# Performance work log

Measured on AMD Instinct MI355X. Metric: run time of the kernel, lower is better.

## Reference

```python
import jax, jax.numpy as jnp
import numpy as np

B = 131072   # batch_sz
NB = 3       # n_blocks (n_agents)
SS = 16      # single_state
NA = 9       # n_action
VD = 128     # vector_dim
CM = 10      # confidence_mid_dim
EPS = 1e-8   # torch CosineSimilarity eps


def _linear_params(k, out_d, in_d):
    bound = 1.0 / np.sqrt(in_d)
    kw, kb = jax.random.split(k)
    W = jax.random.uniform(kw, (out_d, in_d), minval=-bound, maxval=bound, dtype=jnp.float32)
    b = jax.random.uniform(kb, (out_d,), minval=-bound, maxval=bound, dtype=jnp.float32)
    return W, b


def setup_inputs() -> dict:
    key = jax.random.key(0)
    ks = jax.random.split(key, 11)
    Wq, bq = _linear_params(ks[0], VD, SS + NA)
    Wk, bk = _linear_params(ks[1], VD, SS + NA)
    Wv, bv = _linear_params(ks[2], VD, SS + NA)
    W1, b1 = _linear_params(ks[3], VD, VD)
    W2, b2 = _linear_params(ks[4], SS, VD)
    Wc1, bc1 = _linear_params(ks[5], CM, NB * (SS + NA))
    Wc2, bc2 = _linear_params(ks[6], 3, CM)
    states = jax.random.normal(ks[7], (B, NB, SS), dtype=jnp.float32)
    action = jax.random.normal(ks[8], (B, NA), dtype=jnp.float32)
    block_id = jax.random.randint(ks[9], (B, NB), 0, 2, dtype=jnp.int32)
    return {
        'states': states, 'action': action, 'block_id': block_id,
        'Wq': Wq, 'bq': bq, 'Wk': Wk, 'bk': bk, 'Wv': Wv, 'bv': bv,
        'W1': W1, 'b1': b1, 'W2': W2, 'b2': b2,
        'Wc1': Wc1, 'bc1': bc1, 'Wc2': Wc2, 'bc2': bc2,
    }


def reference(states, action, block_id, Wq, bq, Wk, bk, Wv, bv, W1, b1, W2, b2, Wc1, bc1, Wc2, bc2):
    # create_block_action: broadcast action over blocks, mask non-selected blocks to -1
    act = jnp.where(block_id[:, :, None] == 1, action[:, None, :], -1.0)  # [B,NB,NA]
    ba = jnp.concatenate([states, act], axis=-1)                          # [B,NB,SS+NA]

    # QKV projections (fused over blocks instead of per-block loop)
    q = ba @ Wq.T + bq   # [B,NB,VD]
    k = ba @ Wk.T + bk
    v = ba @ Wv.T + bv

    # cosine-similarity attention: d[b,i,j] = cos(q[b,i], k[b,j])
    num = jnp.einsum('bid,bjd->bij', q, k)                                # [B,NB,NB]
    qn = jnp.linalg.norm(q, axis=-1)                                      # [B,NB]
    kn = jnp.linalg.norm(k, axis=-1)
    d = num / jnp.maximum(qn[:, :, None] * kn[:, None, :], EPS)
    a = jax.nn.softmax(d, axis=2)

    res = jnp.einsum('bij,bjd->bid', a, v)                                # [B,NB,VD]
    res = jnp.tanh(res @ W1.T + b1)
    res = res @ W2.T + b2                                                 # [B,NB,SS]
    res = res.reshape(B, 1, NB * SS)

    flat = ba.reshape(B, 1, NB * (SS + NA))                               # [B,1,75]
    conf = jax.nn.sigmoid(jax.nn.sigmoid(flat @ Wc1.T + bc1) @ Wc2.T + bc2)  # [B,1,3]

    residuals = jnp.concatenate([res, conf], axis=-1)                     # [B,1,51]
    base = jnp.concatenate(
        [states.reshape(B, 1, NB * SS), jnp.zeros((B, 1, 3), dtype=states.dtype)], axis=-1)
    return base + residuals
```

## Files before the change

kernel.cpp:

```cpp
#include <hip/hip_runtime.h>
#include <math.h>

#define BTOT 131072
#define NBK 3
#define SS 16
#define NA 9
#define BAD 25
#define STR 28
#define VD 128
#define CM 10
#define OUTD 51
#define EPS 1e-8f

#define O_GQK  0
#define O_GQQ  700
#define O_GKK  1400
#define O_V1   2100
#define O_V2   2128
#define O_VQ   2156
#define O_VK   2184
#define O_C    2212
#define O_M    2216
#define O_B2   7976
#define O_WC1  7992
#define O_BC1  8832
#define O_WC2  8844
#define O_BC2  8880
#define LDS_F  8884
#define O_PKM  LDS_F
#define O_PKW2 (LDS_F + 2048)
#define PKM_N  4096
#define PKW2_N 2048

#define NDOT  (O_M + PKM_N)
#define NCOPY (16 + 840 + 12 + 36 + 4 + PKW2_N)

typedef __attribute__((ext_vector_type(8))) short short8;
typedef __attribute__((ext_vector_type(4))) float floatx4;

__device__ __forceinline__ float fast_sigmoid(float x) {
    return __builtin_amdgcn_rcpf(1.0f + __expf(-x));
}

__device__ __forceinline__ unsigned short f2bf(float f) {
    unsigned int u = __float_as_uint(f);
    u += 0x7FFFu + ((u >> 16) & 1u);
    return (unsigned short)(u >> 16);
}

__global__ __launch_bounds__(256) void prep_dots(
    const float* __restrict__ Wq, const float* __restrict__ bq,
    const float* __restrict__ Wk, const float* __restrict__ bk,
    const float* __restrict__ Wv, const float* __restrict__ bv,
    const float* __restrict__ W1, const float* __restrict__ b1,
    float* __restrict__ ws) {
    int lane = threadIdx.x & 63;
    int gidx = blockIdx.x * 4 + (threadIdx.x >> 6);
    if (gidx >= NDOT) return;

    const float* pa = bq;  const float* pb = bk;
    int sa = 1, sb = 1;
    float scale = 1.0f, bias = 0.0f;
    bool zero = false;
    bool isbf = false; int bfpos = 0;

    if (gidx < O_M) {
        int idx = gidx;
        if (idx < O_GQQ) {
            int e = idx / STR, f = idx % STR;
            if (f < BAD) { pa = Wq + e; sa = BAD; pb = Wk + f; sb = BAD; }
            else zero = true;
        } else if (idx < O_GKK) {
            int j = idx - O_GQQ; int e = j / STR, f = j % STR;
            if (f < BAD && f <= e) { pa = Wq + e; sa = BAD; pb = Wq + f; sb = BAD; scale = (f == e) ? 1.0f : 2.0f; }
            else zero = true;
        } else if (idx < O_V1) {
            int j = idx - O_GKK; int e = j / STR, f = j % STR;
            if (f < BAD && f <= e) { pa = Wk + e; sa = BAD; pb = Wk + f; sb = BAD; scale = (f == e) ? 1.0f : 2.0f; }
            else zero = true;
        } else if (idx < O_V2) {
            int e = idx - O_V1;
            if (e < BAD) { pa = Wq + e; sa = BAD; pb = bk; }
            else zero = true;
        } else if (idx < O_VQ) {
            int e = idx - O_V2;
            if (e < BAD) { pa = Wk + e; sa = BAD; pb = bq; }
            else zero = true;
        } else if (idx < O_VK) {
            int e = idx - O_VQ;
            if (e < BAD) { pa = Wq + e; sa = BAD; pb = bq; }
            else zero = true;
        } else if (idx < O_C) {
            int e = idx - O_VK;
            if (e < BAD) { pa = Wk + e; sa = BAD; pb = bk; }
            else zero = true;
        } else {
            int j = idx - O_C;
            if (j == 0)      { pa = bq; pb = bk; }
            else if (j == 1) { pa = bq; pb = bq; }
            else if (j == 2) { pa = bk; pb = bk; }
            else zero = true;
        }
    } else {
        int p = gidx - O_M;
        isbf = true; bfpos = p;
        int l2 = (p >> 3) & 63, j = p & 7;
        int n = (p >> 9) * 16 + (l2 & 15);
        int k = ((l2 >> 4) << 3) + j;
        if (k < BAD)       { pa = W1 + n * VD; pb = Wv + k; sb = BAD; scale = 2.0f; }
        else if (k == BAD) { pa = W1 + n * VD; pb = bv; scale = 2.0f; bias = 2.0f * b1[n]; }
        else zero = true;
    }

    float s = 0.0f;
    if (!zero)
        s = pa[sa * lane] * pb[sb * lane] + pa[sa * (lane + 64)] * pb[sb * (lane + 64)];
    #pragma unroll
    for (int off = 1; off < 64; off <<= 1) s += __shfl_xor(s, off);
    float val = zero ? 0.0f : (s * scale + bias);
    if (lane == 0) {
        if (isbf) ((unsigned short*)(ws + O_PKM))[bfpos] = f2bf(val);
        else ws[gidx] = val;
    }
}

__global__ __launch_bounds__(256) void prep_copy(
    const float* __restrict__ W2, const float* __restrict__ b2,
    const float* __restrict__ Wc1, const float* __restrict__ bc1,
    const float* __restrict__ Wc2, const float* __restrict__ bc2,
    float* __restrict__ ws) {
    int c = blockIdx.x * 256 + threadIdx.x;
    if (c >= NCOPY) return;
    if (c < 16) { ws[O_B2 + c] = b2[c]; return; }
    c -= 16;
    if (c < 840) {
        int m = c / 84, r = c % 84, i = r / STR, f = r % STR;
        ws[O_WC1 + c] = (f < BAD) ? Wc1[m * (NBK * BAD) + i * BAD + f] : 0.0f;
        return;
    }
    c -= 840;
    if (c < 12) { ws[O_BC1 + c] = (c < CM) ? bc1[c] : 0.0f; return; }
    c -= 12;
    if (c < 36) { int o = c / 12, mm = c % 12; ws[O_WC2 + c] = (mm < CM) ? Wc2[o * CM + mm] : 0.0f; return; }
    c -= 36;
    if (c < 4) { ws[O_BC2 + c] = (c < 3) ? bc2[c] : 0.0f; return; }
    c -= 4;
    int kt = c >> 9, l = (c >> 3) & 63, j = c & 7;
    int o = l & 15;
    int k = kt * 32 + ((l >> 4) << 3) + j;
    ((unsigned short*)(ws + O_PKW2))[c] = f2bf(W2[o * VD + k]);
}

__global__ __launch_bounds__(256) void main_kernel(
    const float* __restrict__ states, const float* __restrict__ action,
    const int* __restrict__ block_id,
    const float* __restrict__ ws, float* __restrict__ out) {
    __shared__ __align__(16) unsigned short At[384 * 40];

    int t = threadIdx.x;
    int lane = t & 63;
    int h = t & 1;
    int le = t >> 1;
    long elem = (long)blockIdx.x * 128 + le;

    const float* st = states + elem * (NBK * SS);
    const float* ac = action + elem * NA;
    const int* bid = block_id + elem * NBK;

    float ba[NBK * BAD];
    #pragma unroll
    for (int i = 0; i < NBK; ++i) {
        const float4* s4 = (const float4*)(st + i * SS);
        #pragma unroll
        for (int w4 = 0; w4 < 4; ++w4) {
            float4 v = s4[w4];
            ba[i * BAD + w4 * 4 + 0] = v.x;
            ba[i * BAD + w4 * 4 + 1] = v.y;
            ba[i * BAD + w4 * 4 + 2] = v.z;
            ba[i * BAD + w4 * 4 + 3] = v.w;
        }
        bool sel = (bid[i] == 1);
        #pragma unroll
        for (int c = 0; c < NA; ++c)
            ba[i * BAD + SS + c] = sel ? ac[c] : -1.0f;
    }

    {
        const float* wc = ws + O_WC1 + h * 5 * 84;
        const float* bc = ws + O_BC1 + h * 5;
        float hp[5];
        #pragma unroll
        for (int k = 0; k < 5; ++k) {
            float s = bc[k];
            #pragma unroll
            for (int i = 0; i < NBK; ++i)
                #pragma unroll
                for (int f = 0; f < BAD; ++f)
                    s += wc[k * 84 + i * STR + f] * ba[i * BAD + f];
            hp[k] = fast_sigmoid(s);
        }
        float op5[5];
        #pragma unroll
        for (int k = 0; k < 5; ++k) op5[k] = __shfl_xor(hp[k], 1);
        if (h == 0) {
            float* op = out + elem * OUTD;
            #pragma unroll
            for (int o = 0; o < 3; ++o) {
                float s = ws[O_BC2 + o];
                #pragma unroll
                for (int m = 0; m < 5; ++m) s += ws[O_WC2 + o * 12 + m] * hp[m];
                #pragma unroll
                for (int m = 0; m < 5; ++m) s += ws[O_WC2 + o * 12 + 5 + m] * op5[m];
                op[48 + o] = fast_sigmoid(s);
            }
        }
    }

    float sl[NBK], dd[NBK];
    {
        const float* vA = ws + (h ? O_V2 : O_V1);
        const float* vB = ws + (h ? O_VK : O_VQ);
        #pragma unroll
        for (int p = 0; p < NBK; ++p) {
            float sA = 0.f, sB = 0.f;
            #pragma unroll
            for (int e = 0; e < BAD; ++e) {
                float b = ba[p * BAD + e];
                sA = fmaf(vA[e], b, sA);
                sB = fmaf(vB[e], b, sB);
            }
            sl[p] = sA; dd[p] = sB;
        }
    }

    float nm[NBK][NBK] = {{0.f,0.f,0.f},{0.f,0.f,0.f},{0.f,0.f,0.f}};
    {
        const float* gq = ws + O_GQK + h * STR;
        #pragma unroll
        for (int i13 = 0; i13 < 13; ++i13) {
            const float* grow = (i13 == 12) ? (ws + O_GQK + 24 * STR)
                                            : (gq + i13 * 2 * STR);
            float t0 = 0.f, t1 = 0.f, t2 = 0.f;
            #pragma unroll
            for (int f = 0; f < BAD; ++f) {
                float g = grow[f];
                t0 = fmaf(g, ba[0 * BAD + f], t0);
                t1 = fmaf(g, ba[1 * BAD + f], t1);
                t2 = fmaf(g, ba[2 * BAD + f], t2);
            }
            float zs = (i13 == 12) ? (1.0f - (float)h) : 1.0f;
            #pragma unroll
            for (int i = 0; i < NBK; ++i) {
                float be;
                if (i13 == 12) be = ba[i * BAD + 24] * zs;
                else {
                    float b_even = ba[i * BAD + 2 * i13];
                    float b_odd  = ba[i * BAD + 2 * i13 + 1];
                    be = h ? b_odd : b_even;
                }
                nm[i][0] = fmaf(be, t0, nm[i][0]);
                nm[i][1] = fmaf(be, t1, nm[i][1]);
                nm[i][2] = fmaf(be, t2, nm[i][2]);
            }
        }
        #pragma unroll
        for (int i = 0; i < NBK; ++i)
            #pragma unroll
            for (int j = 0; j < NBK; ++j)
                nm[i][j] += __shfl_xor(nm[i][j], 1);
    }

    float sn2[NBK] = {0.f, 0.f, 0.f};
    {
        const float* gt = ws + (h ? O_GKK : O_GQQ);
        #pragma unroll
        for (int e = 0; e < BAD; ++e) {
            float p0 = 0.f, p1 = 0.f, p2 = 0.f;
            #pragma unroll
            for (int f = 0; f <= e; ++f) {
                float g = gt[e * STR + f];
                p0 = fmaf(g, ba[0 * BAD + f], p0);
                p1 = fmaf(g, ba[1 * BAD + f], p1);
                p2 = fmaf(g, ba[2 * BAD + f], p2);
            }
            sn2[0] = fmaf(ba[0 * BAD + e], p0, sn2[0]);
            sn2[1] = fmaf(ba[1 * BAD + e], p1, sn2[1]);
            sn2[2] = fmaf(ba[2 * BAD + e], p2, sn2[2]);
        }
    }
    float c0 = ws[O_C + 0];
    float cc = ws[O_C + 1 + h];
    float rn[NBK];
    #pragma unroll
    for (int p = 0; p < NBK; ++p) {
        sn2[p] += 2.0f * dd[p] + cc;
        rn[p] = __builtin_amdgcn_sqrtf(fmaxf(sn2[p], 0.0f));
    }

    float orn[NBK], osl[NBK];
    #pragma unroll
    for (int p = 0; p < NBK; ++p) {
        orn[p] = __shfl_xor(rn[p], 1);
        osl[p] = __shfl_xor(sl[p], 1);
    }
    float s1v[NBK], s2v[NBK], qv[NBK], kv[NBK];
    #pragma unroll
    for (int p = 0; p < NBK; ++p) {
        s1v[p] = h ? osl[p] : sl[p];
        s2v[p] = h ? sl[p] : osl[p];
        qv[p]  = h ? orn[p] : rn[p];
        kv[p]  = h ? rn[p] : orn[p];
    }

    float att[NBK][NBK];
    #pragma unroll
    for (int i = 0; i < NBK; ++i) {
        float dv[NBK];
        #pragma unroll
        for (int j = 0; j < NBK; ++j)
            dv[j] = (nm[i][j] + s1v[i] + s2v[j] + c0) *
                    __builtin_amdgcn_rcpf(fmaxf(qv[i] * kv[j], EPS));
        float mx = fmaxf(dv[0], fmaxf(dv[1], dv[2]));
        float e0 = __expf(dv[0] - mx);
        float e1 = __expf(dv[1] - mx);
        float e2 = __expf(dv[2] - mx);
        float inv = __builtin_amdgcn_rcpf(e0 + e1 + e2);
        att[i][0] = e0 * inv;
        att[i][1] = e1 * inv;
        att[i][2] = e2 * inv;
    }

    #pragma unroll
    for (int i = 0; i < NBK; ++i) {
        unsigned int* dst = (unsigned int*)&At[(le * 3 + i) * 40];
        #pragma unroll
        for (int d = 0; d < 6; ++d) {
            float a_lo = ba[0 * BAD + 2 * d]     * att[i][0] + ba[1 * BAD + 2 * d]     * att[i][1] + ba[2 * BAD + 2 * d]     * att[i][2];
            float a_hi = ba[0 * BAD + 2 * d + 1] * att[i][0] + ba[1 * BAD + 2 * d + 1] * att[i][1] + ba[2 * BAD + 2 * d + 1] * att[i][2];
            float b_lo = ba[0 * BAD + 12 + 2 * d]     * att[i][0] + ba[1 * BAD + 12 + 2 * d]     * att[i][1] + ba[2 * BAD + 12 + 2 * d]     * att[i][2];
            float b_hi = ba[0 * BAD + 12 + 2 * d + 1] * att[i][0] + ba[1 * BAD + 12 + 2 * d + 1] * att[i][1] + ba[2 * BAD + 12 + 2 * d + 1] * att[i][2];
            float v_lo = h ? b_lo : a_lo;
            float v_hi = h ? b_hi : a_hi;
            dst[h * 6 + d] = (unsigned int)f2bf(v_lo) | ((unsigned int)f2bf(v_hi) << 16);
        }
        if (h) {
            float v24 = ba[0 * BAD + 24] * att[i][0] + ba[1 * BAD + 24] * att[i][1] + ba[2 * BAD + 24] * att[i][2];
            dst[12] = (unsigned int)f2bf(v24) | (0x3F80u << 16);
        } else {
            dst[13] = 0u; dst[14] = 0u; dst[15] = 0u;
        }
    }

    asm volatile("s_waitcnt lgkmcnt(0)" ::: "memory");

    {
        int w = t >> 6;
        int m = lane & 15, q = lane >> 4;
        const short8* pkM = (const short8*)(ws + O_PKM);
        const short8* pkW2 = (const short8*)(ws + O_PKW2);
        float b2v = ws[O_B2 + m];
        long blockbase = (long)blockIdx.x * 128;
        int addrA = ((q & 1) ? (m + 32) : m) << 2;
        int addrB = addrA + 64;
        bool hiSel = (q >= 2);

        for (int tt = 0; tt < 6; ++tt) {
            int tile = w * 6 + tt;
            short8 af = *(const short8*)&At[(tile * 16 + m) * 40 + q * 8];
            floatx4 accT[8];
            #pragma unroll
            for (int nt = 0; nt < 8; ++nt) {
                floatx4 z = {0.f, 0.f, 0.f, 0.f};
                accT[nt] = __builtin_amdgcn_mfma_f32_16x16x32_bf16(pkM[nt * 64 + lane], af, z, 0, 0, 0);
            }
            unsigned int pk[8][2];
            #pragma unroll
            for (int nt = 0; nt < 8; ++nt) {
                float x0 = fmaf(-2.0f, __builtin_amdgcn_rcpf(1.0f + __expf(accT[nt][0])), 1.0f);
                float x1 = fmaf(-2.0f, __builtin_amdgcn_rcpf(1.0f + __expf(accT[nt][1])), 1.0f);
                float x2 = fmaf(-2.0f, __builtin_amdgcn_rcpf(1.0f + __expf(accT[nt][2])), 1.0f);
                float x3 = fmaf(-2.0f, __builtin_amdgcn_rcpf(1.0f + __expf(accT[nt][3])), 1.0f);
                asm("v_cvt_pk_bf16_f32 %0, %1, %2" : "=v"(pk[nt][0]) : "v"(x0), "v"(x1));
                asm("v_cvt_pk_bf16_f32 %0, %1, %2" : "=v"(pk[nt][1]) : "v"(x2), "v"(x3));
            }
            floatx4 acc2 = {0.f, 0.f, 0.f, 0.f};
            #pragma unroll
            for (int kt = 0; kt < 4; ++kt) {
                int lo0 = __builtin_amdgcn_ds_bpermute(addrA, (int)pk[2 * kt][0]);
                int hi0 = __builtin_amdgcn_ds_bpermute(addrA, (int)pk[2 * kt + 1][0]);
                int lo1 = __builtin_amdgcn_ds_bpermute(addrA, (int)pk[2 * kt][1]);
                int hi1 = __builtin_amdgcn_ds_bpermute(addrA, (int)pk[2 * kt + 1][1]);
                int lo2 = __builtin_amdgcn_ds_bpermute(addrB, (int)pk[2 * kt][0]);
                int hi2 = __builtin_amdgcn_ds_bpermute(addrB, (int)pk[2 * kt + 1][0]);
                int lo3 = __builtin_amdgcn_ds_bpermute(addrB, (int)pk[2 * kt][1]);
                int hi3 = __builtin_amdgcn_ds_bpermute(addrB, (int)pk[2 * kt + 1][1]);
                union { unsigned int u[4]; short8 s; } a2u;
                a2u.u[0] = (unsigned int)(hiSel ? hi0 : lo0);
                a2u.u[1] = (unsigned int)(hiSel ? hi1 : lo1);
                a2u.u[2] = (unsigned int)(hiSel ? hi2 : lo2);
                a2u.u[3] = (unsigned int)(hiSel ? hi3 : lo3);
                acc2 = __builtin_amdgcn_mfma_f32_16x16x32_bf16(a2u.s, pkW2[kt * 64 + lane], acc2, 0, 0, 0);
            }
            #pragma unroll
            for (int rr = 0; rr < 4; ++rr) {
                int lrow = tile * 16 + q * 4 + rr;
                int et = lrow / 3, i = lrow - et * 3;
                long ge = blockbase + et;
                float base = states[ge * 48 + i * 16 + m];
                out[ge * OUTD + i * 16 + m] = acc2[rr] + base + b2v;
            }
        }
    }
}

extern "C" void kernel_launch(void* const* d_in, const int* in_sizes, int n_in,
                              void* d_out, int out_size, void* d_ws, size_t ws_size,
                              hipStream_t stream) {
    const float* states = (const float*)d_in[0];
    const float* action = (const float*)d_in[1];
    const int* block_id = (const int*)d_in[2];
    const float* Wq = (const float*)d_in[3];
    const float* bq = (const float*)d_in[4];
    const float* Wk = (const float*)d_in[5];
    const float* bk = (const float*)d_in[6];
    const float* Wv = (const float*)d_in[7];
    const float* bv = (const float*)d_in[8];
    const float* W1 = (const float*)d_in[9];
    const float* b1 = (const float*)d_in[10];
    const float* W2 = (const float*)d_in[11];
    const float* b2 = (const float*)d_in[12];
    const float* Wc1 = (const float*)d_in[13];
    const float* bc1 = (const float*)d_in[14];
    const float* Wc2 = (const float*)d_in[15];
    const float* bc2 = (const float*)d_in[16];
    float* out = (float*)d_out;
    float* ws = (float*)d_ws;

    hipLaunchKernelGGL(prep_dots, dim3((NDOT + 3) / 4), dim3(256), 0, stream,
                       Wq, bq, Wk, bk, Wv, bv, W1, b1, ws);
    hipLaunchKernelGGL(prep_copy, dim3((NCOPY + 255) / 256), dim3(256), 0, stream,
                       W2, b2, Wc1, bc1, Wc2, bc2, ws);
    hipLaunchKernelGGL(main_kernel, dim3(BTOT / 128), dim3(256), 0, stream,
                       states, action, block_id, ws, out);
}
```

Baseline: 167.8 us.

## Split element work across waves instead of lane pairs, exchange via LDS

Each element's two halves of work move from adjacent lanes to two different wavefronts. The half index is now wave-uniform, so branches are uniform and weight loads become scalar. Partial results that used to pass through shuffles now go through shared memory with block barriers. Blocks shrink to 128 threads covering 64 elements each, which adds LDS traffic and barriers and halves the per-block tile count.

```diff
diff --git a/kernel.cpp b/kernel.cpp
--- a/kernel.cpp
+++ b/kernel.cpp
@@ -151,17 +151,16 @@
     ((unsigned short*)(ws + O_PKW2))[c] = f2bf(W2[o * VD + k]);
 }
 
-__global__ __launch_bounds__(256) void main_kernel(
+__global__ __launch_bounds__(128) void main_kernel(
     const float* __restrict__ states, const float* __restrict__ action,
     const int* __restrict__ block_id,
     const float* __restrict__ ws, float* __restrict__ out) {
-    __shared__ __align__(16) unsigned short At[384 * 40];
+    __shared__ __align__(16) unsigned short At[192 * 40];
 
     int t = threadIdx.x;
     int lane = t & 63;
-    int h = t & 1;
-    int le = t >> 1;
-    long elem = (long)blockIdx.x * 128 + le;
+    int h_u = __builtin_amdgcn_readfirstlane(t >> 6);
+    long elem = (long)blockIdx.x * 64 + lane;
 
     const float* st = states + elem * (NBK * SS);
     const float* ac = action + elem * NA;
@@ -185,10 +184,10 @@
             ba[i * BAD + SS + c] = sel ? ac[c] : -1.0f;
     }
 
-    {
-        const float* wc = ws + O_WC1 + h * 5 * 84;
-        const float* bc = ws + O_BC1 + h * 5;
-        float hp[5];
+    float hp[5];
+    {
+        const float* wc = ws + O_WC1 + h_u * 5 * 84;
+        const float* bc = ws + O_BC1 + h_u * 5;
         #pragma unroll
         for (int k = 0; k < 5; ++k) {
             float s = bc[k];
@@ -199,27 +198,12 @@
                     s += wc[k * 84 + i * STR + f] * ba[i * BAD + f];
             hp[k] = fast_sigmoid(s);
         }
-        float op5[5];
-        #pragma unroll
-        for (int k = 0; k < 5; ++k) op5[k] = __shfl_xor(hp[k], 1);
-        if (h == 0) {
-            float* op = out + elem * OUTD;
-            #pragma unroll
-            for (int o = 0; o < 3; ++o) {
-                float s = ws[O_BC2 + o];
-                #pragma unroll
-                for (int m = 0; m < 5; ++m) s += ws[O_WC2 + o * 12 + m] * hp[m];
-                #pragma unroll
-                for (int m = 0; m < 5; ++m) s += ws[O_WC2 + o * 12 + 5 + m] * op5[m];
-                op[48 + o] = fast_sigmoid(s);
-            }
-        }
     }
 
     float sl[NBK], dd[NBK];
     {
-        const float* vA = ws + (h ? O_V2 : O_V1);
-        const float* vB = ws + (h ? O_VK : O_VQ);
+        const float* vA = ws + (h_u ? O_V2 : O_V1);
+        const float* vB = ws + (h_u ? O_VK : O_VQ);
         #pragma unroll
         for (int p = 0; p < NBK; ++p) {
             float sA = 0.f, sB = 0.f;
@@ -234,12 +218,11 @@
     }
 
     float nm[NBK][NBK] = {{0.f,0.f,0.f},{0.f,0.f,0.f},{0.f,0.f,0.f}};
-    {
-        const float* gq = ws + O_GQK + h * STR;
-        #pragma unroll
-        for (int i13 = 0; i13 < 13; ++i13) {
-            const float* grow = (i13 == 12) ? (ws + O_GQK + 24 * STR)
-                                            : (gq + i13 * 2 * STR);
+    if (h_u == 0) {
+        #pragma unroll
+        for (int ii = 0; ii < 13; ++ii) {
+            const int e = (ii < 12) ? (2 * ii) : 24;
+            const float* grow = ws + O_GQK + e * STR;
             float t0 = 0.f, t1 = 0.f, t2 = 0.f;
             #pragma unroll
             for (int f = 0; f < BAD; ++f) {
@@ -248,31 +231,41 @@
                 t1 = fmaf(g, ba[1 * BAD + f], t1);
                 t2 = fmaf(g, ba[2 * BAD + f], t2);
             }
-            float zs = (i13 == 12) ? (1.0f - (float)h) : 1.0f;
             #pragma unroll
             for (int i = 0; i < NBK; ++i) {
-                float be;
-                if (i13 == 12) be = ba[i * BAD + 24] * zs;
-                else {
-                    float b_even = ba[i * BAD + 2 * i13];
-                    float b_odd  = ba[i * BAD + 2 * i13 + 1];
-                    be = h ? b_odd : b_even;
-                }
+                float be = ba[i * BAD + e];
                 nm[i][0] = fmaf(be, t0, nm[i][0]);
                 nm[i][1] = fmaf(be, t1, nm[i][1]);
                 nm[i][2] = fmaf(be, t2, nm[i][2]);
             }
         }
-        #pragma unroll
-        for (int i = 0; i < NBK; ++i)
-            #pragma unroll
-            for (int j = 0; j < NBK; ++j)
-                nm[i][j] += __shfl_xor(nm[i][j], 1);
-    }
-
-    float sn2[NBK] = {0.f, 0.f, 0.f};
-    {
-        const float* gt = ws + (h ? O_GKK : O_GQQ);
+    } else {
+        #pragma unroll
+        for (int ii = 0; ii < 12; ++ii) {
+            const int e = 2 * ii + 1;
+            const float* grow = ws + O_GQK + e * STR;
+            float t0 = 0.f, t1 = 0.f, t2 = 0.f;
+            #pragma unroll
+            for (int f = 0; f < BAD; ++f) {
+                float g = grow[f];
+                t0 = fmaf(g, ba[0 * BAD + f], t0);
+                t1 = fmaf(g, ba[1 * BAD + f], t1);
+                t2 = fmaf(g, ba[2 * BAD + f], t2);
+            }
+            #pragma unroll
+            for (int i = 0; i < NBK; ++i) {
+                float be = ba[i * BAD + e];
+                nm[i][0] = fmaf(be, t0, nm[i][0]);
+                nm[i][1] = fmaf(be, t1, nm[i][1]);
+                nm[i][2] = fmaf(be, t2, nm[i][2]);
+            }
+        }
+    }
+
+    float rn[NBK];
+    {
+        const float* gt = ws + (h_u ? O_GKK : O_GQQ);
+        float sn2[NBK] = {0.f, 0.f, 0.f};
         #pragma unroll
         for (int e = 0; e < BAD; ++e) {
             float p0 = 0.f, p1 = 0.f, p2 = 0.f;
@@ -287,30 +280,66 @@
             sn2[1] = fmaf(ba[1 * BAD + e], p1, sn2[1]);
             sn2[2] = fmaf(ba[2 * BAD + e], p2, sn2[2]);
         }
-    }
-    float c0 = ws[O_C + 0];
-    float cc = ws[O_C + 1 + h];
-    float rn[NBK];
-    #pragma unroll
-    for (int p = 0; p < NBK; ++p) {
-        sn2[p] += 2.0f * dd[p] + cc;
-        rn[p] = __builtin_amdgcn_sqrtf(fmaxf(sn2[p], 0.0f));
-    }
-
-    float orn[NBK], osl[NBK];
-    #pragma unroll
-    for (int p = 0; p < NBK; ++p) {
-        orn[p] = __shfl_xor(rn[p], 1);
-        osl[p] = __shfl_xor(sl[p], 1);
-    }
+        float cc = ws[O_C + 1 + h_u];
+        #pragma unroll
+        for (int p = 0; p < NBK; ++p) {
+            sn2[p] += 2.0f * dd[p] + cc;
+            rn[p] = __builtin_amdgcn_sqrtf(fmaxf(sn2[p], 0.0f));
+        }
+    }
+
+    float* exf = (float*)At;
+    {
+        float* my = exf + (h_u * 64 + lane) * 21;
+        my[0] = rn[0]; my[1] = rn[1]; my[2] = rn[2];
+        my[3] = sl[0]; my[4] = sl[1]; my[5] = sl[2];
+        #pragma unroll
+        for (int i = 0; i < NBK; ++i)
+            #pragma unroll
+            for (int j = 0; j < NBK; ++j)
+                my[6 + i * 3 + j] = nm[i][j];
+        #pragma unroll
+        for (int k = 0; k < 5; ++k) my[15 + k] = hp[k];
+    }
+    __syncthreads();
+
+    float orn[NBK], osl[NBK], ohp[5];
+    {
+        const float* ot = exf + ((1 - h_u) * 64 + lane) * 21;
+        orn[0] = ot[0]; orn[1] = ot[1]; orn[2] = ot[2];
+        osl[0] = ot[3]; osl[1] = ot[4]; osl[2] = ot[5];
+        #pragma unroll
+        for (int i = 0; i < NBK; ++i)
+            #pragma unroll
+            for (int j = 0; j < NBK; ++j)
+                nm[i][j] += ot[6 + i * 3 + j];
+        #pragma unroll
+        for (int k = 0; k < 5; ++k) ohp[k] = ot[15 + k];
+    }
+    __syncthreads();
+
+    if (h_u == 0) {
+        float* op = out + elem * OUTD;
+        #pragma unroll
+        for (int o = 0; o < 3; ++o) {
+            float s = ws[O_BC2 + o];
+            #pragma unroll
+            for (int m = 0; m < 5; ++m) s += ws[O_WC2 + o * 12 + m] * hp[m];
+            #pragma unroll
+            for (int m = 0; m < 5; ++m) s += ws[O_WC2 + o * 12 + 5 + m] * ohp[m];
+            op[48 + o] = fast_sigmoid(s);
+        }
+    }
+
     float s1v[NBK], s2v[NBK], qv[NBK], kv[NBK];
     #pragma unroll
     for (int p = 0; p < NBK; ++p) {
-        s1v[p] = h ? osl[p] : sl[p];
-        s2v[p] = h ? sl[p] : osl[p];
-        qv[p]  = h ? orn[p] : rn[p];
-        kv[p]  = h ? rn[p] : orn[p];
-    }
+        s1v[p] = h_u ? osl[p] : sl[p];
+        s2v[p] = h_u ? sl[p] : osl[p];
+        qv[p]  = h_u ? orn[p] : rn[p];
+        kv[p]  = h_u ? rn[p] : orn[p];
+    }
+    float c0 = ws[O_C + 0];
 
     float att[NBK][NBK];
     #pragma unroll
@@ -330,42 +359,47 @@
         att[i][2] = e2 * inv;
     }
 
-    #pragma unroll
-    for (int i = 0; i < NBK; ++i) {
-        unsigned int* dst = (unsigned int*)&At[(le * 3 + i) * 40];
-        #pragma unroll
-        for (int d = 0; d < 6; ++d) {
-            float a_lo = ba[0 * BAD + 2 * d]     * att[i][0] + ba[1 * BAD + 2 * d]     * att[i][1] + ba[2 * BAD + 2 * d]     * att[i][2];
-            float a_hi = ba[0 * BAD + 2 * d + 1] * att[i][0] + ba[1 * BAD + 2 * d + 1] * att[i][1] + ba[2 * BAD + 2 * d + 1] * att[i][2];
-            float b_lo = ba[0 * BAD + 12 + 2 * d]     * att[i][0] + ba[1 * BAD + 12 + 2 * d]     * att[i][1] + ba[2 * BAD + 12 + 2 * d]     * att[i][2];
-            float b_hi = ba[0 * BAD + 12 + 2 * d + 1] * att[i][0] + ba[1 * BAD + 12 + 2 * d + 1] * att[i][1] + ba[2 * BAD + 12 + 2 * d + 1] * att[i][2];
-            float v_lo = h ? b_lo : a_lo;
-            float v_hi = h ? b_hi : a_hi;
-            dst[h * 6 + d] = (unsigned int)f2bf(v_lo) | ((unsigned int)f2bf(v_hi) << 16);
-        }
-        if (h) {
+    if (h_u == 0) {
+        #pragma unroll
+        for (int i = 0; i < NBK; ++i) {
+            unsigned int* dst = (unsigned int*)&At[(lane * 3 + i) * 40];
+            #pragma unroll
+            for (int d = 0; d < 6; ++d) {
+                float lo = ba[0 * BAD + 2 * d]     * att[i][0] + ba[1 * BAD + 2 * d]     * att[i][1] + ba[2 * BAD + 2 * d]     * att[i][2];
+                float hi = ba[0 * BAD + 2 * d + 1] * att[i][0] + ba[1 * BAD + 2 * d + 1] * att[i][1] + ba[2 * BAD + 2 * d + 1] * att[i][2];
+                dst[d] = (unsigned int)f2bf(lo) | ((unsigned int)f2bf(hi) << 16);
+            }
+            dst[13] = 0u; dst[14] = 0u; dst[15] = 0u;
+        }
+    } else {
+        #pragma unroll
+        for (int i = 0; i < NBK; ++i) {
+            unsigned int* dst = (unsigned int*)&At[(lane * 3 + i) * 40];
+            #pragma unroll
+            for (int d = 0; d < 6; ++d) {
+                float lo = ba[0 * BAD + 12 + 2 * d]     * att[i][0] + ba[1 * BAD + 12 + 2 * d]     * att[i][1] + ba[2 * BAD + 12 + 2 * d]     * att[i][2];
+                float hi = ba[0 * BAD + 12 + 2 * d + 1] * att[i][0] + ba[1 * BAD + 12 + 2 * d + 1] * att[i][1] + ba[2 * BAD + 12 + 2 * d + 1] * att[i][2];
+                dst[6 + d] = (unsigned int)f2bf(lo) | ((unsigned int)f2bf(hi) << 16);
+            }
             float v24 = ba[0 * BAD + 24] * att[i][0] + ba[1 * BAD + 24] * att[i][1] + ba[2 * BAD + 24] * att[i][2];
             dst[12] = (unsigned int)f2bf(v24) | (0x3F80u << 16);
-        } else {
-            dst[13] = 0u; dst[14] = 0u; dst[15] = 0u;
-        }
-    }
-
-    asm volatile("s_waitcnt lgkmcnt(0)" ::: "memory");
-
-    {
-        int w = t >> 6;
+        }
+    }
+
+    __syncthreads();
+
+    {
         int m = lane & 15, q = lane >> 4;
         const short8* pkM = (const short8*)(ws + O_PKM);
         const short8* pkW2 = (const short8*)(ws + O_PKW2);
         float b2v = ws[O_B2 + m];
-        long blockbase = (long)blockIdx.x * 128;
+        long blockbase = (long)blockIdx.x * 64;
         int addrA = ((q & 1) ? (m + 32) : m) << 2;
         int addrB = addrA + 64;
         bool hiSel = (q >= 2);
 
         for (int tt = 0; tt < 6; ++tt) {
-            int tile = w * 6 + tt;
+            int tile = h_u * 6 + tt;
             short8 af = *(const short8*)&At[(tile * 16 + m) * 40 + q * 8];
             floatx4 accT[8];
             #pragma unroll
@@ -440,6 +474,6 @@
                        Wq, bq, Wk, bk, Wv, bv, W1, b1, ws);
     hipLaunchKernelGGL(prep_copy, dim3((NCOPY + 255) / 256), dim3(256), 0, stream,
                        W2, b2, Wc1, bc1, Wc2, bc2, ws);
-    hipLaunchKernelGGL(main_kernel, dim3(BTOT / 128), dim3(256), 0, stream,
+    hipLaunchKernelGGL(main_kernel, dim3(BTOT / 64), dim3(128), 0, stream,
                        states, action, block_id, ws, out);
 }
```

Measured after the change: 171.8 us. 2.4% more time.
